# Optimization experiments

Measured on AMD Instinct MI355X. Metric: run time of the kernel, lower is better.

Reference implementation:

```python
import jax, jax.numpy as jnp
from jax import lax
import numpy as np

B, T, D, H = 64, 2048, 256, 256


def setup_inputs() -> dict:
    key = jax.random.key(0)
    k1, k2, k3 = jax.random.split(key, 3)
    s_x = 1.0 / np.sqrt(D)
    s_h = 1.0 / np.sqrt(H)
    return {
        "inputs": jax.random.normal(k1, (B, T, D), dtype=jnp.float32),
        "hidden": jnp.zeros((1, B, H), dtype=jnp.float32),
        "Wx": jax.random.normal(k2, (3 * H, D), dtype=jnp.float32) * s_x,
        "bx": jnp.zeros((3 * H,), dtype=jnp.float32),
        "Wh": jax.random.normal(k3, (3 * H, H), dtype=jnp.float32) * s_h,
        "bh": jnp.zeros((3 * H,), dtype=jnp.float32),
    }


def reference(inputs, hidden, Wx, bx, Wh, bh):
    # inputs: [B, T, D]; hidden: [1, B, H] (leading 1 broadcast, as in the torch code)
    def step(h, x_t):
        # x_t: [B, 3H] (precomputed x2h); h: [1, B, H]
        h_t = h[0] @ Wh.T + bh                      # [B, 3H] (h2h + squeeze)
        x_r, x_u, x_n = jnp.split(x_t, 3, axis=1)
        h_r, h_u, h_n = jnp.split(h_t, 3, axis=1)
        reset = jax.nn.sigmoid(x_r + h_r)
        upd = jax.nn.sigmoid(x_u + h_u)
        new = jnp.tanh(x_n + reset * h_n)
        hy = upd * h + (1.0 - upd) * new            # broadcasts to [1, B, H]
        return hy, hy[0]

    # Hoist the input projection out of the scan (same math, one big GEMM).
    xs = jnp.einsum('btd,gd->btg', inputs, Wx) + bx  # [B, T, 3H]
    xs = jnp.transpose(xs, (1, 0, 2))                # [T, B, 3H]
    _, hs = lax.scan(step, hidden, xs)               # hs: [T, B, H]
    return jnp.transpose(hs, (1, 0, 2))              # [B, T, H]
```

## Files before the change

kernel.cpp:

```cpp
#include <hip/hip_runtime.h>
#include <hip/hip_fp16.h>

#define B_SZ 64
#define T_SZ 2048
#define D_SZ 256
#define H_SZ 256
#define G3   768
#define M_SZ (B_SZ * T_SZ)

typedef _Float16 half2v __attribute__((ext_vector_type(2)));
typedef _Float16 half4v __attribute__((ext_vector_type(4)));
typedef _Float16 half8v __attribute__((ext_vector_type(8)));
typedef float    f32x4  __attribute__((ext_vector_type(4)));

static __device__ __forceinline__ float fdot2f(uint a, uint b, float acc) {
#if __has_builtin(__builtin_amdgcn_fdot2)
  return __builtin_amdgcn_fdot2(__builtin_bit_cast(half2v, a),
                                __builtin_bit_cast(half2v, b), acc, false);
#else
  half2v av = __builtin_bit_cast(half2v, a), bv = __builtin_bit_cast(half2v, b);
  acc = fmaf((float)av[0], (float)bv[0], acc);
  acc = fmaf((float)av[1], (float)bv[1], acc);
  return acc;
#endif
}

static __device__ __forceinline__ float h2f(ushort u) {
  return (float)__builtin_bit_cast(_Float16, u);
}
static __device__ __forceinline__ ushort f2h(float x) {
  return __builtin_bit_cast(ushort, (_Float16)x);
}

__global__ void prep_w(const float* __restrict__ Wx, const float* __restrict__ Wh,
                       ushort* __restrict__ Wxh, ushort* __restrict__ Whh) {
  int i = blockIdx.x * 256 + threadIdx.x;
  if (i < G3 * D_SZ) {
    Wxh[i] = f2h(Wx[i]);
    Whh[i] = f2h(Wh[i]);
  }
}

__global__ __launch_bounds__(256) void gemm_x(
    const float* __restrict__ A,
    const ushort* __restrict__ Bw,
    const float* __restrict__ bx,
    ushort* __restrict__ xs) {
  __shared__ _Float16 As[128][72];
  __shared__ _Float16 Bs[256][72];
  const int nt = blockIdx.x, mt = blockIdx.y;
  const int tid = threadIdx.x;
  const int lane = tid & 63, wv = tid >> 6;
  const int wr = (wv >> 1) * 64, wc = (wv & 1) * 128;
  const int l15 = lane & 15, l4 = lane >> 4;
  f32x4 acc[4][8] = {};
  for (int kt = 0; kt < 4; kt++) {
#pragma unroll
    for (int i = 0; i < 8; i++) {
      int f = tid + i * 256;
      int r = f >> 4, c4 = f & 15;
      float4 v = *(const float4*)(A + (size_t)(mt * 128 + r) * D_SZ + kt * 64 + c4 * 4);
      half4v h;
      h[0] = (_Float16)v.x; h[1] = (_Float16)v.y;
      h[2] = (_Float16)v.z; h[3] = (_Float16)v.w;
      *(half4v*)&As[r][c4 * 4] = h;
    }
#pragma unroll
    for (int i = 0; i < 8; i++) {
      int f = tid + i * 256;
      int r = f >> 3, c8 = f & 7;
      uint4 v = *(const uint4*)(Bw + (size_t)(nt * 256 + r) * D_SZ + kt * 64 + c8 * 8);
      *(uint4*)&Bs[r][c8 * 8] = v;
    }
    __syncthreads();
#pragma unroll
    for (int kk = 0; kk < 2; kk++) {
      half8v af[4], bf[8];
#pragma unroll
      for (int m = 0; m < 4; m++)
        af[m] = *(const half8v*)&As[wr + m * 16 + l15][kk * 32 + l4 * 8];
#pragma unroll
      for (int n = 0; n < 8; n++)
        bf[n] = *(const half8v*)&Bs[wc + n * 16 + l15][kk * 32 + l4 * 8];
#pragma unroll
      for (int m = 0; m < 4; m++) {
#pragma unroll
        for (int n = 0; n < 8; n++) {
          acc[m][n] = __builtin_amdgcn_mfma_f32_16x16x32_f16(af[m], bf[n], acc[m][n], 0, 0, 0);
        }
      }
    }
    __syncthreads();
  }
#pragma unroll
  for (int n = 0; n < 8; n++) {
    int col = nt * 256 + wc + n * 16 + l15;
    float bxv = bx[col];
#pragma unroll
    for (int m = 0; m < 4; m++) {
#pragma unroll
      for (int v4 = 0; v4 < 4; v4++) {
        int row = mt * 128 + wr + m * 16 + l4 * 4 + v4;
        xs[(size_t)row * G3 + col] = f2h(acc[m][n][v4] + bxv);
      }
    }
  }
}

__global__ __launch_bounds__(768) void gru_rec(
    const ushort* __restrict__ xs,
    const ushort* __restrict__ Whh,
    const float* __restrict__ bh,
    const float* __restrict__ hid,
    float* __restrict__ out) {
  const int b = blockIdx.x;
  const int j = threadIdx.x;
  __shared__ alignas(16) ushort h16[H_SZ];
  __shared__ float rs[H_SZ];
  __shared__ float us[H_SZ];

  uint w[128];
  {
    const uint4* wp = (const uint4*)(Whh + (size_t)j * D_SZ);
#pragma unroll
    for (int i = 0; i < 32; i++) {
      uint4 q = wp[i];
      w[4 * i + 0] = q.x; w[4 * i + 1] = q.y;
      w[4 * i + 2] = q.z; w[4 * i + 3] = q.w;
    }
  }
  const float bhj = bh[j];
  if (j < H_SZ) h16[j] = f2h(hid[b * H_SZ + j]);
  __syncthreads();

  const ushort* xrow = xs + (size_t)b * T_SZ * G3 + j;
  float* orow = out + (size_t)b * T_SZ * H_SZ;
  ushort xu = xrow[0];

#pragma unroll 1
  for (int t = 0; t < T_SZ; t++) {
    ushort xnext = (t + 1 < T_SZ) ? xrow[(size_t)(t + 1) * G3] : (ushort)0;
    float x = h2f(xu);

    float d0 = 0.f, d1 = 0.f;
    const uint4* hq = (const uint4*)h16;
#pragma unroll
    for (int c = 0; c < 32; c++) {
      uint4 q = hq[c];
      d0 = fdot2f(w[4 * c + 0], q.x, d0);
      d1 = fdot2f(w[4 * c + 1], q.y, d1);
      d0 = fdot2f(w[4 * c + 2], q.z, d0);
      d1 = fdot2f(w[4 * c + 3], q.w, d1);
    }
    float pre = d0 + d1 + bhj;

    if (j < 512) {
      float a = pre + x;
      float s = 1.f / (1.f + __expf(-a));
      if (j < H_SZ) rs[j] = s;
      else          us[j - H_SZ] = s;
    }
    __syncthreads();

    if (j >= 512) {
      int i = j - 512;
      float r = rs[i], u = us[i];
      float hold = h2f(h16[i]);
      float arg = x + r * pre;
      float e = __expf(-2.f * fabsf(arg));
      float th = copysignf((1.f - e) / (1.f + e), arg);
      float hn = u * hold + (1.f - u) * th;
      orow[(size_t)t * H_SZ + i] = hn;
      h16[i] = f2h(hn);
    }
    __syncthreads();
    xu = xnext;
  }
}

extern "C" void kernel_launch(void* const* d_in, const int* in_sizes, int n_in,
                              void* d_out, int out_size, void* d_ws, size_t ws_size,
                              hipStream_t stream) {
  const float* inp = (const float*)d_in[0];
  const float* hid = (const float*)d_in[1];
  const float* Wx  = (const float*)d_in[2];
  const float* bx  = (const float*)d_in[3];
  const float* Wh  = (const float*)d_in[4];
  const float* bh  = (const float*)d_in[5];
  float* out = (float*)d_out;

  char* ws = (char*)d_ws;
  ushort* xs = (ushort*)ws;
  size_t xs_bytes = (size_t)M_SZ * G3 * sizeof(ushort);
  ushort* Wxh = (ushort*)(ws + xs_bytes);
  ushort* Whh = Wxh + (size_t)G3 * D_SZ;

  prep_w<<<768, 256, 0, stream>>>(Wx, Wh, Wxh, Whh);
  gemm_x<<<dim3(3, 1024), 256, 0, stream>>>(inp, Wxh, bx, xs);
  gru_rec<<<B_SZ, G3, 0, stream>>>(xs, Whh, bh, hid, out);
}
```

Before: 2.584 ms.

## Compute all three GRU gates per thread with double-buffered hidden state

The recurrent kernel now runs 256 threads per batch row instead of 768. Each thread owns one hidden unit and computes its reset, update and new-gate dot products itself, using weights repacked by a new prep kernel into k-pair-major uint layout. This removes the shared-memory exchange of r/u values and one of the two barriers per timestep. The hidden vector is double-buffered so a single barrier suffices, and divisions become hardware reciprocals. The trade-off is 384 weight registers per thread, which risks spilling or AGPR traffic, and a third as many waves left to hide latency.

```diff
diff --git a/kernel.cpp b/kernel.cpp
--- a/kernel.cpp
+++ b/kernel.cpp
@@ -31,14 +31,22 @@
 static __device__ __forceinline__ ushort f2h(float x) {
   return __builtin_bit_cast(ushort, (_Float16)x);
 }
-
-__global__ void prep_w(const float* __restrict__ Wx, const float* __restrict__ Wh,
-                       ushort* __restrict__ Wxh, ushort* __restrict__ Whh) {
+static __device__ __forceinline__ float fast_rcp(float x) {
+  return __builtin_amdgcn_rcpf(x);
+}
+
+__global__ void prep_wx(const float* __restrict__ Wx, ushort* __restrict__ Wxh) {
   int i = blockIdx.x * 256 + threadIdx.x;
-  if (i < G3 * D_SZ) {
-    Wxh[i] = f2h(Wx[i]);
-    Whh[i] = f2h(Wh[i]);
-  }
+  if (i < G3 * D_SZ) Wxh[i] = f2h(Wx[i]);
+}
+
+__global__ void prep_wh(const float* __restrict__ Wh, uint* __restrict__ Wp) {
+  int j = blockIdx.x * 256 + threadIdx.x;
+  int kp = blockIdx.y;
+  float a = Wh[(size_t)j * D_SZ + 2 * kp];
+  float b = Wh[(size_t)j * D_SZ + 2 * kp + 1];
+  uint lo = (uint)f2h(a), hi = (uint)f2h(b);
+  Wp[(size_t)kp * G3 + j] = lo | (hi << 16);
 }
 
 __global__ __launch_bounds__(256) void gemm_x(
@@ -107,74 +115,74 @@
   }
 }
 
-__global__ __launch_bounds__(768) void gru_rec(
+__global__ __launch_bounds__(256, 1) void gru_rec(
     const ushort* __restrict__ xs,
-    const ushort* __restrict__ Whh,
+    const uint* __restrict__ Wp,
     const float* __restrict__ bh,
     const float* __restrict__ hid,
     float* __restrict__ out) {
   const int b = blockIdx.x;
-  const int j = threadIdx.x;
-  __shared__ alignas(16) ushort h16[H_SZ];
-  __shared__ float rs[H_SZ];
-  __shared__ float us[H_SZ];
-
-  uint w[128];
-  {
-    const uint4* wp = (const uint4*)(Whh + (size_t)j * D_SZ);
-#pragma unroll
-    for (int i = 0; i < 32; i++) {
-      uint4 q = wp[i];
-      w[4 * i + 0] = q.x; w[4 * i + 1] = q.y;
-      w[4 * i + 2] = q.z; w[4 * i + 3] = q.w;
-    }
-  }
-  const float bhj = bh[j];
-  if (j < H_SZ) h16[j] = f2h(hid[b * H_SZ + j]);
+  const int i = threadIdx.x;
+  __shared__ alignas(16) ushort hbuf[2][H_SZ];
+
+  uint wr[128], wu[128], wn[128];
+#pragma unroll
+  for (int kp = 0; kp < 128; kp++) {
+    wr[kp] = Wp[(size_t)kp * G3 + i];
+    wu[kp] = Wp[(size_t)kp * G3 + 256 + i];
+    wn[kp] = Wp[(size_t)kp * G3 + 512 + i];
+  }
+  const float bhr = bh[i], bhu = bh[256 + i], bhn = bh[512 + i];
+
+  float hprev = hid[b * H_SZ + i];
+  hbuf[0][i] = f2h(hprev);
   __syncthreads();
 
-  const ushort* xrow = xs + (size_t)b * T_SZ * G3 + j;
-  float* orow = out + (size_t)b * T_SZ * H_SZ;
-  ushort xu = xrow[0];
+  const ushort* xrow = xs + (size_t)b * T_SZ * G3 + i;
+  float* orow = out + (size_t)b * T_SZ * H_SZ + i;
 
 #pragma unroll 1
   for (int t = 0; t < T_SZ; t++) {
-    ushort xnext = (t + 1 < T_SZ) ? xrow[(size_t)(t + 1) * G3] : (ushort)0;
-    float x = h2f(xu);
-
-    float d0 = 0.f, d1 = 0.f;
-    const uint4* hq = (const uint4*)h16;
+    ushort xr16 = xrow[0];
+    ushort xu16 = xrow[256];
+    ushort xn16 = xrow[512];
+    xrow += G3;
+
+    float ar0 = 0.f, ar1 = 0.f, au0 = 0.f, au1 = 0.f, an0 = 0.f, an1 = 0.f;
+    const uint4* hq = (const uint4*)hbuf[t & 1];
 #pragma unroll
     for (int c = 0; c < 32; c++) {
       uint4 q = hq[c];
-      d0 = fdot2f(w[4 * c + 0], q.x, d0);
-      d1 = fdot2f(w[4 * c + 1], q.y, d1);
-      d0 = fdot2f(w[4 * c + 2], q.z, d0);
-      d1 = fdot2f(w[4 * c + 3], q.w, d1);
-    }
-    float pre = d0 + d1 + bhj;
-
-    if (j < 512) {
-      float a = pre + x;
-      float s = 1.f / (1.f + __expf(-a));
-      if (j < H_SZ) rs[j] = s;
-      else          us[j - H_SZ] = s;
-    }
-    __syncthreads();
-
-    if (j >= 512) {
-      int i = j - 512;
-      float r = rs[i], u = us[i];
-      float hold = h2f(h16[i]);
-      float arg = x + r * pre;
-      float e = __expf(-2.f * fabsf(arg));
-      float th = copysignf((1.f - e) / (1.f + e), arg);
-      float hn = u * hold + (1.f - u) * th;
-      orow[(size_t)t * H_SZ + i] = hn;
-      h16[i] = f2h(hn);
-    }
-    __syncthreads();
-    xu = xnext;
+      ar0 = fdot2f(wr[4 * c + 0], q.x, ar0);
+      ar1 = fdot2f(wr[4 * c + 1], q.y, ar1);
+      au0 = fdot2f(wu[4 * c + 0], q.x, au0);
+      au1 = fdot2f(wu[4 * c + 1], q.y, au1);
+      an0 = fdot2f(wn[4 * c + 0], q.x, an0);
+      an1 = fdot2f(wn[4 * c + 1], q.y, an1);
+      ar0 = fdot2f(wr[4 * c + 2], q.z, ar0);
+      ar1 = fdot2f(wr[4 * c + 3], q.w, ar1);
+      au0 = fdot2f(wu[4 * c + 2], q.z, au0);
+      au1 = fdot2f(wu[4 * c + 3], q.w, au1);
+      an0 = fdot2f(wn[4 * c + 2], q.z, an0);
+      an1 = fdot2f(wn[4 * c + 3], q.w, an1);
+    }
+    float pre_r = ar0 + ar1 + bhr;
+    float pre_u = au0 + au1 + bhu;
+    float pre_n = an0 + an1 + bhn;
+
+    float r = fast_rcp(1.f + __expf(-(h2f(xr16) + pre_r)));
+    float u = fast_rcp(1.f + __expf(-(h2f(xu16) + pre_u)));
+    float arg = h2f(xn16) + r * pre_n;
+    float e = __expf(-2.f * fabsf(arg));
+    float th = copysignf((1.f - e) * fast_rcp(1.f + e), arg);
+    float hn = u * hprev + (1.f - u) * th;
+
+    orow[(size_t)t * H_SZ] = hn;
+    hbuf[(t + 1) & 1][i] = f2h(hn);
+    hprev = hn;
+
+    asm volatile("s_waitcnt lgkmcnt(0)" ::: "memory");
+    __builtin_amdgcn_s_barrier();
   }
 }
 
@@ -193,9 +201,10 @@
   ushort* xs = (ushort*)ws;
   size_t xs_bytes = (size_t)M_SZ * G3 * sizeof(ushort);
   ushort* Wxh = (ushort*)(ws + xs_bytes);
-  ushort* Whh = Wxh + (size_t)G3 * D_SZ;
-
-  prep_w<<<768, 256, 0, stream>>>(Wx, Wh, Wxh, Whh);
+  uint* Wp = (uint*)(ws + xs_bytes + (size_t)G3 * D_SZ * sizeof(ushort));
+
+  prep_wx<<<768, 256, 0, stream>>>(Wx, Wxh);
+  prep_wh<<<dim3(3, 128), 256, 0, stream>>>(Wh, Wp);
   gemm_x<<<dim3(3, 1024), 256, 0, stream>>>(inp, Wxh, bx, xs);
-  gru_rec<<<B_SZ, G3, 0, stream>>>(xs, Whh, bh, hid, out);
-}
+  gru_rec<<<B_SZ, 256, 0, stream>>>(xs, Wp, bh, hid, out);
+}
```

New measurement: 5.903 ms. +128.4%, slower.

## Interleave recurrent weights for coalesced loads, add accumulators, lighten barriers

Applied to the files above, without the earlier changes.

Adds a prep kernel that reorders Wh into fp16 pairs interleaved by output row, so each thread loads its register-resident weights coalesced across threads. The dot product now uses four independent accumulators, and the sigmoid and tanh divisions become hardware reciprocals. Full __syncthreads are replaced with an LDS waitcnt plus s_barrier, and launch bounds set an occupancy hint. The reciprocal trades a little accuracy for fewer instructions inside the sequential time loop, which dominates runtime.

```diff
diff --git a/kernel.cpp b/kernel.cpp
--- a/kernel.cpp
+++ b/kernel.cpp
@@ -31,14 +31,25 @@
 static __device__ __forceinline__ ushort f2h(float x) {
   return __builtin_bit_cast(ushort, (_Float16)x);
 }
-
-__global__ void prep_w(const float* __restrict__ Wx, const float* __restrict__ Wh,
-                       ushort* __restrict__ Wxh, ushort* __restrict__ Whh) {
+static __device__ __forceinline__ float fast_rcp(float x) {
+  return __builtin_amdgcn_rcpf(x);
+}
+
+__global__ void prep_wx(const float* __restrict__ Wx, ushort* __restrict__ Wxh) {
   int i = blockIdx.x * 256 + threadIdx.x;
-  if (i < G3 * D_SZ) {
-    Wxh[i] = f2h(Wx[i]);
-    Whh[i] = f2h(Wh[i]);
-  }
+  if (i < G3 * D_SZ) Wxh[i] = f2h(Wx[i]);
+}
+
+__global__ void prep_wq(const float* __restrict__ Wh, uint* __restrict__ Wq) {
+  int f = blockIdx.x * 256 + threadIdx.x;
+  int e = f & 3;
+  int t2 = f >> 2;
+  int j = t2 % G3;
+  int s4 = t2 / G3;
+  int kp = 4 * s4 + e;
+  float a = Wh[(size_t)j * D_SZ + 2 * kp];
+  float b = Wh[(size_t)j * D_SZ + 2 * kp + 1];
+  Wq[f] = (uint)f2h(a) | ((uint)f2h(b) << 16);
 }
 
 __global__ __launch_bounds__(256) void gemm_x(
@@ -107,9 +118,9 @@
   }
 }
 
-__global__ __launch_bounds__(768) void gru_rec(
+__global__ __launch_bounds__(768, 3) void gru_rec(
     const ushort* __restrict__ xs,
-    const ushort* __restrict__ Whh,
+    const uint* __restrict__ Wq,
     const float* __restrict__ bh,
     const float* __restrict__ hid,
     float* __restrict__ out) {
@@ -119,15 +130,11 @@
   __shared__ float rs[H_SZ];
   __shared__ float us[H_SZ];
 
-  uint w[128];
+  uint4 w4[32];
   {
-    const uint4* wp = (const uint4*)(Whh + (size_t)j * D_SZ);
-#pragma unroll
-    for (int i = 0; i < 32; i++) {
-      uint4 q = wp[i];
-      w[4 * i + 0] = q.x; w[4 * i + 1] = q.y;
-      w[4 * i + 2] = q.z; w[4 * i + 3] = q.w;
-    }
+    const uint4* wp = (const uint4*)Wq;
+#pragma unroll
+    for (int s4 = 0; s4 < 32; s4++) w4[s4] = wp[(size_t)s4 * G3 + j];
   }
   const float bhj = bh[j];
   if (j < H_SZ) h16[j] = f2h(hid[b * H_SZ + j]);
@@ -142,25 +149,27 @@
     ushort xnext = (t + 1 < T_SZ) ? xrow[(size_t)(t + 1) * G3] : (ushort)0;
     float x = h2f(xu);
 
-    float d0 = 0.f, d1 = 0.f;
+    float d0 = 0.f, d1 = 0.f, d2 = 0.f, d3 = 0.f;
     const uint4* hq = (const uint4*)h16;
 #pragma unroll
     for (int c = 0; c < 32; c++) {
       uint4 q = hq[c];
-      d0 = fdot2f(w[4 * c + 0], q.x, d0);
-      d1 = fdot2f(w[4 * c + 1], q.y, d1);
-      d0 = fdot2f(w[4 * c + 2], q.z, d0);
-      d1 = fdot2f(w[4 * c + 3], q.w, d1);
-    }
-    float pre = d0 + d1 + bhj;
+      uint4 wv = w4[c];
+      d0 = fdot2f(wv.x, q.x, d0);
+      d1 = fdot2f(wv.y, q.y, d1);
+      d2 = fdot2f(wv.z, q.z, d2);
+      d3 = fdot2f(wv.w, q.w, d3);
+    }
+    float pre = ((d0 + d1) + (d2 + d3)) + bhj;
 
     if (j < 512) {
       float a = pre + x;
-      float s = 1.f / (1.f + __expf(-a));
+      float s = fast_rcp(1.f + __expf(-a));
       if (j < H_SZ) rs[j] = s;
       else          us[j - H_SZ] = s;
     }
-    __syncthreads();
+    asm volatile("s_waitcnt lgkmcnt(0)" ::: "memory");
+    __builtin_amdgcn_s_barrier();
 
     if (j >= 512) {
       int i = j - 512;
@@ -168,12 +177,13 @@
       float hold = h2f(h16[i]);
       float arg = x + r * pre;
       float e = __expf(-2.f * fabsf(arg));
-      float th = copysignf((1.f - e) / (1.f + e), arg);
+      float th = copysignf((1.f - e) * fast_rcp(1.f + e), arg);
       float hn = u * hold + (1.f - u) * th;
       orow[(size_t)t * H_SZ + i] = hn;
       h16[i] = f2h(hn);
     }
-    __syncthreads();
+    asm volatile("s_waitcnt lgkmcnt(0)" ::: "memory");
+    __builtin_amdgcn_s_barrier();
     xu = xnext;
   }
 }
@@ -193,9 +203,10 @@
   ushort* xs = (ushort*)ws;
   size_t xs_bytes = (size_t)M_SZ * G3 * sizeof(ushort);
   ushort* Wxh = (ushort*)(ws + xs_bytes);
-  ushort* Whh = Wxh + (size_t)G3 * D_SZ;
-
-  prep_w<<<768, 256, 0, stream>>>(Wx, Wh, Wxh, Whh);
+  uint* Wq = (uint*)(ws + xs_bytes + (size_t)G3 * D_SZ * sizeof(ushort));
+
+  prep_wx<<<768, 256, 0, stream>>>(Wx, Wxh);
+  prep_wq<<<384, 256, 0, stream>>>(Wh, Wq);
   gemm_x<<<dim3(3, 1024), 256, 0, stream>>>(inp, Wxh, bx, xs);
-  gru_rec<<<B_SZ, G3, 0, stream>>>(xs, Whh, bh, hid, out);
-}
+  gru_rec<<<B_SZ, G3, 0, stream>>>(xs, Wq, bh, hid, out);
+}
```

Measured after the change: 2.509 ms, median of 2. 1.03x faster.
